# Kernel tuning notes

Measured on AMD Instinct MI355X. Metric: run time of the kernel, lower is better.

Reference implementation:

```python
import jax, jax.numpy as jnp
import numpy as np


def _haar_filters():
    s = 1.0 / np.sqrt(2.0).astype(np.float32)
    l = jnp.array([s, s], dtype=jnp.float32)
    h = jnp.array([-s, s], dtype=jnp.float32)
    ll = jnp.outer(l, l)
    lh = jnp.outer(h, l)
    hl = jnp.outer(l, h)
    hh = jnp.outer(h, h)
    # module registers ll, -lh, -hl, hh as buffers
    return ll, -lh, -hl, hh


def setup_inputs() -> dict:
    key = jax.random.key(0)
    x = jax.random.normal(key, (16, 12, 512, 512), dtype=jnp.float32)
    fll, flh, fhl, fhh = _haar_filters()
    return {"x": x, "fll": fll, "flh": flh, "fhl": fhl, "fhh": fhh}


def _upfirdn_band(x, f):
    # upfirdn2d(band, f, up_factor=2, padding=(1,0,1,0)):
    #   2) zero pad: 1 on left of W, 1 on top of H
    #   3) valid conv with 2x2 FIR filter, applied per channel
    #   4) down_factor=1 interpolate -> identity
    B, C, H, W = x.shape
    up = jax.image.resize(x, (B, C, 2 * H, 2 * W), method="bilinear")
    p = jnp.pad(up, ((0, 0), (0, 0), (1, 0), (1, 0)))  # [B,C,2H+1,2W+1]
    w = jnp.tile(f[None, None].astype(x.dtype), (C, 1, 1, 1))  # depthwise [C,1,2,2]
    return jax.lax.conv_general_dilated(
        p, w, window_strides=(1, 1), padding="VALID",
        feature_group_count=C,
        dimension_numbers=("NCHW", "OIHW", "NCHW"),
    )  # [B,C,2H,2W]


def reference(x, fll, flh, fhl, fhh):
    ll, lh, hl, hh = jnp.split(x, 4, axis=1)  # input.chunk(4, 1)
    out = (_upfirdn_band(ll, fll)
           + _upfirdn_band(lh, flh)
           + _upfirdn_band(hl, fhl)
           + _upfirdn_band(hh, fhh))
    return out
```

## Files before the change

kernel.cpp:

```cpp
#include <hip/hip_runtime.h>

namespace {

constexpr int Hh = 512, Ww = 512, OH = 1024, OW = 1024;
constexpr int NB_Y = 256;
constexpr int NBC  = 48;
constexpr int NWG  = NB_Y * NBC;

typedef float f32x4 __attribute__((ext_vector_type(4)));

__global__ __launch_bounds__(256) void ihaar(
    const float* __restrict__ x,
    const float* __restrict__ f0,
    const float* __restrict__ f1,
    const float* __restrict__ f2,
    const float* __restrict__ f3,
    float* __restrict__ out)
{
  const int bid = blockIdx.x;
  const int wg  = (bid & 7) * (NWG / 8) + (bid >> 3);
  const int bc   = wg / NB_Y;
  const int yblk = wg - bc * NB_Y;
  const int b = bc / 3;
  const int c = bc - 3 * b;

  const int t    = threadIdx.x;
  const int lane = t & 63;
  const int wv   = t >> 6;
  const int half = wv & 1;
  const int ty   = wv >> 1;
  const int y    = 2 * yblk + ty;
  const int x0   = half * 256 + lane * 4;

  const float4 F[4] = { *(const float4*)f0, *(const float4*)f1,
                        *(const float4*)f2, *(const float4*)f3 };

  const int u0r = (y > 0) ? y - 1 : 0;
  const int u2r = (y < Hh - 1) ? y + 1 : y;

  const bool needL = (lane == 0)  && (half == 1);
  const bool needR = (lane == 63) && (half == 0);
  const bool le = (x0 == 0), re = (x0 == Ww - 4);

  float e0=0.f,e1=0.f,e2=0.f,e3=0.f,e4=0.f,e5=0.f,e6=0.f,e7=0.f;
  float o0=0.f,o1=0.f,o2=0.f,o3=0.f,o4=0.f,o5=0.f,o6=0.f,o7=0.f;

#pragma unroll
  for (int g = 0; g < 4; ++g) {
    const float* Xp = x + (size_t)(b * 12 + g * 3 + c) * (Hh * Ww);
    const float4 q0 = *(const float4*)(Xp + (size_t)u0r * Ww + x0);
    const float4 q1 = *(const float4*)(Xp + (size_t)y   * Ww + x0);
    const float4 q2 = *(const float4*)(Xp + (size_t)u2r * Ww + x0);
    float s0 = 0.f, s1 = 0.f, s2 = 0.f;
    if (needL || needR) {
      const int sc = needL ? (x0 - 1) : (x0 + 4);
      s0 = Xp[(size_t)u0r * Ww + sc];
      s1 = Xp[(size_t)y   * Ww + sc];
      s2 = Xp[(size_t)u2r * Ww + sc];
    }

    const float f00 = F[g].x, f01 = F[g].y, f10 = F[g].z;
    const float uu0 = f00, uu1 = f10;
    const float vv1 = f01 * __builtin_amdgcn_rcpf(f00);

    float pa0, pa1, pb0, pb1, pb2;
    if (y > 0) { pa0 = 0.75f*uu0 + 0.25f*uu1; pa1 = 0.25f*uu0 + 0.75f*uu1; }
    else       { pa0 = 0.f;                   pa1 = uu1; }
    if (y == 0)           { pb0 = 0.f;         pb1 = uu0 + 0.75f*uu1;   pb2 = 0.25f*uu1; }
    else if (y == Hh - 1) { pb0 = 0.25f*uu0;   pb1 = 0.75f*uu0 + uu1;   pb2 = 0.f; }
    else                  { pb0 = 0.25f*uu0;   pb1 = 0.75f*(uu0+uu1);   pb2 = 0.25f*uu1; }

    const float Ve0 = pa0*q0.x + pa1*q1.x;
    const float Ve1 = pa0*q0.y + pa1*q1.y;
    const float Ve2 = pa0*q0.z + pa1*q1.z;
    const float Ve3 = pa0*q0.w + pa1*q1.w;
    const float Vo0 = pb0*q0.x + pb1*q1.x + pb2*q2.x;
    const float Vo1 = pb0*q0.y + pb1*q1.y + pb2*q2.y;
    const float Vo2 = pb0*q0.z + pb1*q1.z + pb2*q2.z;
    const float Vo3 = pb0*q0.w + pb1*q1.w + pb2*q2.w;

    float VeM = __shfl_up(Ve3, 1);
    float VoM = __shfl_up(Vo3, 1);
    float VeP = __shfl_down(Ve0, 1);
    float VoP = __shfl_down(Vo0, 1);
    if (needL) { VeM = pa0*s0 + pa1*s1; VoM = pb0*s0 + pb1*s1 + pb2*s2; }
    if (needR) { VeP = pa0*s0 + pa1*s1; VoP = pb0*s0 + pb1*s1 + pb2*s2; }

    const float h0i = 0.75f + 0.25f*vv1;
    const float h1i = 0.25f + 0.75f*vv1;
    const float g0i = 0.25f;
    const float g1i = 0.75f*(1.f + vv1);
    const float g2i = 0.25f*vv1;
    const float h0a = le ? 0.f : h0i;
    const float h1a = le ? vv1 : h1i;
    const float g0a = le ? 0.f : g0i;
    const float g1a = le ? (1.f + 0.75f*vv1) : g1i;
    const float g1d = re ? (0.75f + vv1) : g1i;
    const float g2d = re ? 0.f : g2i;

    e0 += h0a*VeM + h1a*Ve0;
    e1 += g0a*VeM + g1a*Ve0 + g2i*Ve1;
    o0 += h0a*VoM + h1a*Vo0;
    o1 += g0a*VoM + g1a*Vo0 + g2i*Vo1;
    e2 += h0i*Ve0 + h1i*Ve1;
    e3 += g0i*Ve0 + g1i*Ve1 + g2i*Ve2;
    o2 += h0i*Vo0 + h1i*Vo1;
    o3 += g0i*Vo0 + g1i*Vo1 + g2i*Vo2;
    e4 += h0i*Ve1 + h1i*Ve2;
    e5 += g0i*Ve1 + g1i*Ve2 + g2i*Ve3;
    o4 += h0i*Vo1 + h1i*Vo2;
    o5 += g0i*Vo1 + g1i*Vo2 + g2i*Vo3;
    e6 += h0i*Ve2 + h1i*Ve3;
    e7 += g0i*Ve2 + g1d*Ve3 + g2d*VeP;
    o6 += h0i*Vo2 + h1i*Vo3;
    o7 += g0i*Vo2 + g1d*Vo3 + g2d*VoP;
  }

  float* op = out + ((size_t)bc * OH + 2 * y) * OW + 2 * x0;
  const f32x4 E0 = { e0, e1, e2, e3 };
  const f32x4 E1 = { e4, e5, e6, e7 };
  const f32x4 O0 = { o0, o1, o2, o3 };
  const f32x4 O1 = { o4, o5, o6, o7 };
  __builtin_nontemporal_store(E0, (f32x4*)op);
  __builtin_nontemporal_store(E1, (f32x4*)(op + 4));
  __builtin_nontemporal_store(O0, (f32x4*)(op + OW));
  __builtin_nontemporal_store(O1, (f32x4*)(op + OW + 4));
}

}

extern "C" void kernel_launch(void* const* d_in, const int* in_sizes, int n_in,
                              void* d_out, int out_size, void* d_ws, size_t ws_size,
                              hipStream_t stream) {
  const float* x   = (const float*)d_in[0];
  const float* fll = (const float*)d_in[1];
  const float* flh = (const float*)d_in[2];
  const float* fhl = (const float*)d_in[3];
  const float* fhh = (const float*)d_in[4];
  float* out = (float*)d_out;

  ihaar<<<dim3(NWG), 256, 0, stream>>>(x, fll, flh, fhl, fhh, out);
}
```

Measured before the change: 77.24 us.

## Share horizontal pass between bands with equal horizontal filter ratio

Each band's vertical interpolation is now summed into one of two accumulator groups, P for bands 0-1 and Q for bands 2-3. The horizontal upsample, filter and shuffle stage then runs once per group instead of once per band, which cuts cross-lane shuffles and horizontal FMAs roughly in half. This relies on bands 0 and 1, and bands 2 and 3, having the same horizontal tap ratio. That holds for Haar filters built as outer products, but the kernel now quietly assumes that filter structure. The kernel appears bandwidth-bound, so the ALU savings may barely show.

```diff
diff --git a/kernel.cpp b/kernel.cpp
--- a/kernel.cpp
+++ b/kernel.cpp
@@ -37,84 +37,83 @@
 
   const int u0r = (y > 0) ? y - 1 : 0;
   const int u2r = (y < Hh - 1) ? y + 1 : y;
-
   const bool needL = (lane == 0)  && (half == 1);
   const bool needR = (lane == 63) && (half == 0);
   const bool le = (x0 == 0), re = (x0 == Ww - 4);
+  const int sc = needL ? (x0 - 1) : (x0 + 4);
 
-  float e0=0.f,e1=0.f,e2=0.f,e3=0.f,e4=0.f,e5=0.f,e6=0.f,e7=0.f;
-  float o0=0.f,o1=0.f,o2=0.f,o3=0.f,o4=0.f,o5=0.f,o6=0.f,o7=0.f;
+  float Pe0=0.f,Pe1=0.f,Pe2=0.f,Pe3=0.f, Po0=0.f,Po1=0.f,Po2=0.f,Po3=0.f;
+  float Qe0=0.f,Qe1=0.f,Qe2=0.f,Qe3=0.f, Qo0=0.f,Qo1=0.f,Qo2=0.f,Qo3=0.f;
+  float SPe=0.f,SPo=0.f,SQe=0.f,SQo=0.f;
 
-#pragma unroll
-  for (int g = 0; g < 4; ++g) {
-    const float* Xp = x + (size_t)(b * 12 + g * 3 + c) * (Hh * Ww);
-    const float4 q0 = *(const float4*)(Xp + (size_t)u0r * Ww + x0);
-    const float4 q1 = *(const float4*)(Xp + (size_t)y   * Ww + x0);
-    const float4 q2 = *(const float4*)(Xp + (size_t)u2r * Ww + x0);
-    float s0 = 0.f, s1 = 0.f, s2 = 0.f;
-    if (needL || needR) {
-      const int sc = needL ? (x0 - 1) : (x0 + 4);
-      s0 = Xp[(size_t)u0r * Ww + sc];
-      s1 = Xp[(size_t)y   * Ww + sc];
-      s2 = Xp[(size_t)u2r * Ww + sc];
-    }
+#define BAND(g, Ae0,Ae1,Ae2,Ae3, Ao0,Ao1,Ao2,Ao3, Se, So) { \
+    const float uu0 = F[g].x, uu1 = F[g].z; \
+    float pa0, pa1, pb0, pb1, pb2; \
+    if (y > 0) { pa0 = 0.75f*uu0 + 0.25f*uu1; pa1 = 0.25f*uu0 + 0.75f*uu1; } \
+    else       { pa0 = 0.f;                   pa1 = uu1; } \
+    if (y == 0)           { pb0 = 0.f;         pb1 = uu0 + 0.75f*uu1; pb2 = 0.25f*uu1; } \
+    else if (y == Hh - 1) { pb0 = 0.25f*uu0;   pb1 = 0.75f*uu0 + uu1; pb2 = 0.f; } \
+    else                  { pb0 = 0.25f*uu0;   pb1 = 0.75f*(uu0+uu1); pb2 = 0.25f*uu1; } \
+    const float* Xp = x + (size_t)(b * 12 + (g) * 3 + c) * (Hh * Ww); \
+    const f32x4 q0 = *(const f32x4*)(Xp + (size_t)u0r * Ww + x0); \
+    const f32x4 q1 = *(const f32x4*)(Xp + (size_t)y   * Ww + x0); \
+    const f32x4 q2 = *(const f32x4*)(Xp + (size_t)u2r * Ww + x0); \
+    Ae0 += pa0*q0.x + pa1*q1.x;  Ae1 += pa0*q0.y + pa1*q1.y; \
+    Ae2 += pa0*q0.z + pa1*q1.z;  Ae3 += pa0*q0.w + pa1*q1.w; \
+    Ao0 += pb0*q0.x + pb1*q1.x + pb2*q2.x; \
+    Ao1 += pb0*q0.y + pb1*q1.y + pb2*q2.y; \
+    Ao2 += pb0*q0.z + pb1*q1.z + pb2*q2.z; \
+    Ao3 += pb0*q0.w + pb1*q1.w + pb2*q2.w; \
+    if (needL || needR) { \
+      const float s0 = Xp[(size_t)u0r * Ww + sc]; \
+      const float s1 = Xp[(size_t)y   * Ww + sc]; \
+      const float s2 = Xp[(size_t)u2r * Ww + sc]; \
+      Se += pa0*s0 + pa1*s1;  So += pb0*s0 + pb1*s1 + pb2*s2; \
+    } \
+  }
 
-    const float f00 = F[g].x, f01 = F[g].y, f10 = F[g].z;
-    const float uu0 = f00, uu1 = f10;
-    const float vv1 = f01 * __builtin_amdgcn_rcpf(f00);
+  BAND(0, Pe0,Pe1,Pe2,Pe3, Po0,Po1,Po2,Po3, SPe, SPo)
+  BAND(1, Pe0,Pe1,Pe2,Pe3, Po0,Po1,Po2,Po3, SPe, SPo)
+  BAND(2, Qe0,Qe1,Qe2,Qe3, Qo0,Qo1,Qo2,Qo3, SQe, SQo)
+  BAND(3, Qe0,Qe1,Qe2,Qe3, Qo0,Qo1,Qo2,Qo3, SQe, SQo)
+#undef BAND
 
-    float pa0, pa1, pb0, pb1, pb2;
-    if (y > 0) { pa0 = 0.75f*uu0 + 0.25f*uu1; pa1 = 0.25f*uu0 + 0.75f*uu1; }
-    else       { pa0 = 0.f;                   pa1 = uu1; }
-    if (y == 0)           { pb0 = 0.f;         pb1 = uu0 + 0.75f*uu1;   pb2 = 0.25f*uu1; }
-    else if (y == Hh - 1) { pb0 = 0.25f*uu0;   pb1 = 0.75f*uu0 + uu1;   pb2 = 0.f; }
-    else                  { pb0 = 0.25f*uu0;   pb1 = 0.75f*(uu0+uu1);   pb2 = 0.25f*uu1; }
+  float PeL = __shfl_up(Pe3, 1),  PoL = __shfl_up(Po3, 1);
+  float QeL = __shfl_up(Qe3, 1),  QoL = __shfl_up(Qo3, 1);
+  float PeR = __shfl_down(Pe0, 1), PoR = __shfl_down(Po0, 1);
+  float QeR = __shfl_down(Qe0, 1), QoR = __shfl_down(Qo0, 1);
+  if (needL) { PeL = SPe; PoL = SPo; QeL = SQe; QoL = SQo; }
+  if (needR) { PeR = SPe; PoR = SPo; QeR = SQe; QoR = SQo; }
 
-    const float Ve0 = pa0*q0.x + pa1*q1.x;
-    const float Ve1 = pa0*q0.y + pa1*q1.y;
-    const float Ve2 = pa0*q0.z + pa1*q1.z;
-    const float Ve3 = pa0*q0.w + pa1*q1.w;
-    const float Vo0 = pb0*q0.x + pb1*q1.x + pb2*q2.x;
-    const float Vo1 = pb0*q0.y + pb1*q1.y + pb2*q2.y;
-    const float Vo2 = pb0*q0.z + pb1*q1.z + pb2*q2.z;
-    const float Vo3 = pb0*q0.w + pb1*q1.w + pb2*q2.w;
+  const float vp = F[0].y * __builtin_amdgcn_rcpf(F[0].x);
+  const float vq = F[2].y * __builtin_amdgcn_rcpf(F[2].x);
+  const float h0p = 0.75f + 0.25f*vp, h1p = 0.25f + 0.75f*vp;
+  const float g0p = 0.25f, g1p = 0.75f*(1.f + vp), g2p = 0.25f*vp;
+  const float h0q = 0.75f + 0.25f*vq, h1q = 0.25f + 0.75f*vq;
+  const float g0q = 0.25f, g1q = 0.75f*(1.f + vq), g2q = 0.25f*vq;
+  const float h0pa = le ? 0.f : h0p, h1pa = le ? vp : h1p;
+  const float g0pa = le ? 0.f : g0p, g1pa = le ? (1.f + 0.75f*vp) : g1p;
+  const float g1pd = re ? (0.75f + vp) : g1p, g2pd = re ? 0.f : g2p;
+  const float h0qa = le ? 0.f : h0q, h1qa = le ? vq : h1q;
+  const float g0qa = le ? 0.f : g0q, g1qa = le ? (1.f + 0.75f*vq) : g1q;
+  const float g1qd = re ? (0.75f + vq) : g1q, g2qd = re ? 0.f : g2q;
 
-    float VeM = __shfl_up(Ve3, 1);
-    float VoM = __shfl_up(Vo3, 1);
-    float VeP = __shfl_down(Ve0, 1);
-    float VoP = __shfl_down(Vo0, 1);
-    if (needL) { VeM = pa0*s0 + pa1*s1; VoM = pb0*s0 + pb1*s1 + pb2*s2; }
-    if (needR) { VeP = pa0*s0 + pa1*s1; VoP = pb0*s0 + pb1*s1 + pb2*s2; }
-
-    const float h0i = 0.75f + 0.25f*vv1;
-    const float h1i = 0.25f + 0.75f*vv1;
-    const float g0i = 0.25f;
-    const float g1i = 0.75f*(1.f + vv1);
-    const float g2i = 0.25f*vv1;
-    const float h0a = le ? 0.f : h0i;
-    const float h1a = le ? vv1 : h1i;
-    const float g0a = le ? 0.f : g0i;
-    const float g1a = le ? (1.f + 0.75f*vv1) : g1i;
-    const float g1d = re ? (0.75f + vv1) : g1i;
-    const float g2d = re ? 0.f : g2i;
-
-    e0 += h0a*VeM + h1a*Ve0;
-    e1 += g0a*VeM + g1a*Ve0 + g2i*Ve1;
-    o0 += h0a*VoM + h1a*Vo0;
-    o1 += g0a*VoM + g1a*Vo0 + g2i*Vo1;
-    e2 += h0i*Ve0 + h1i*Ve1;
-    e3 += g0i*Ve0 + g1i*Ve1 + g2i*Ve2;
-    o2 += h0i*Vo0 + h1i*Vo1;
-    o3 += g0i*Vo0 + g1i*Vo1 + g2i*Vo2;
-    e4 += h0i*Ve1 + h1i*Ve2;
-    e5 += g0i*Ve1 + g1i*Ve2 + g2i*Ve3;
-    o4 += h0i*Vo1 + h1i*Vo2;
-    o5 += g0i*Vo1 + g1i*Vo2 + g2i*Vo3;
-    e6 += h0i*Ve2 + h1i*Ve3;
-    e7 += g0i*Ve2 + g1d*Ve3 + g2d*VeP;
-    o6 += h0i*Vo2 + h1i*Vo3;
-    o7 += g0i*Vo2 + g1d*Vo3 + g2d*VoP;
-  }
+  const float e0 = h0pa*PeL + h1pa*Pe0           + h0qa*QeL + h1qa*Qe0;
+  const float e1 = g0pa*PeL + g1pa*Pe0 + g2p*Pe1 + g0qa*QeL + g1qa*Qe0 + g2q*Qe1;
+  const float e2 = h0p*Pe0  + h1p*Pe1            + h0q*Qe0  + h1q*Qe1;
+  const float e3 = g0p*Pe0  + g1p*Pe1  + g2p*Pe2 + g0q*Qe0  + g1q*Qe1  + g2q*Qe2;
+  const float e4 = h0p*Pe1  + h1p*Pe2            + h0q*Qe1  + h1q*Qe2;
+  const float e5 = g0p*Pe1  + g1p*Pe2  + g2p*Pe3 + g0q*Qe1  + g1q*Qe2  + g2q*Qe3;
+  const float e6 = h0p*Pe2  + h1p*Pe3            + h0q*Qe2  + h1q*Qe3;
+  const float e7 = g0p*Pe2  + g1pd*Pe3 + g2pd*PeR+ g0q*Qe2  + g1qd*Qe3 + g2qd*QeR;
+  const float o0 = h0pa*PoL + h1pa*Po0           + h0qa*QoL + h1qa*Qo0;
+  const float o1 = g0pa*PoL + g1pa*Po0 + g2p*Po1 + g0qa*QoL + g1qa*Qo0 + g2q*Qo1;
+  const float o2 = h0p*Po0  + h1p*Po1            + h0q*Qo0  + h1q*Qo1;
+  const float o3 = g0p*Po0  + g1p*Po1  + g2p*Po2 + g0q*Qo0  + g1q*Qo1  + g2q*Qo2;
+  const float o4 = h0p*Po1  + h1p*Po2            + h0q*Qo1  + h1q*Qo2;
+  const float o5 = g0p*Po1  + g1p*Po2  + g2p*Po3 + g0q*Qo1  + g1q*Qo2  + g2q*Qo3;
+  const float o6 = h0p*Po2  + h1p*Po3            + h0q*Qo2  + h1q*Qo3;
+  const float o7 = g0p*Po2  + g1pd*Po3 + g2pd*PoR+ g0q*Qo2  + g1qd*Qo3 + g2qd*QoR;
 
   float* op = out + ((size_t)bc * OH + 2 * y) * OW + 2 * x0;
   const f32x4 E0 = { e0, e1, e2, e3 };
```

New measurement: 68.11 us. -11.8%, faster.
